# Performance work log

Hardware: AMD Instinct MI355X
Metric: run time of the kernel (lower is better)

Reference implementation:

```python
import jax, jax.numpy as jnp
import numpy as np

KH, KW = 3, 3
T_MIN, T_MAX = 0.0, 1.0  # default layer params (set_params never called)


def setup_inputs() -> dict:
    key = jax.random.key(0)
    k1, k2, k3 = jax.random.split(key, 3)
    # spike times in [0, 1]
    tj = jax.random.uniform(k1, (16, 258, 258), dtype=jnp.float32)
    # (filters, 1, kh, kw), scaled so outputs are not all clamped at t_max
    kernel = jax.random.normal(k2, (128, 1, KH, KW), dtype=jnp.float32) * 0.05
    D_i = jax.random.normal(k3, (9, 128), dtype=jnp.float32) * 0.01
    return {"tj": tj, "kernel": kernel, "D_i": D_i}


def reference(tj, kernel, D_i):
    # tj: [B, S, S]; valid padding, default branch (BN buffer == 0).
    B, S, _ = tj.shape
    Hv = S - KH + 1  # image_valid_size
    Fc = kernel.shape[0]
    # torch: W = kernel.view(-1, filters) -> row-major reinterpretation of (F,1,kh,kw) as (9, F)
    W = kernel.reshape(KH * KW, Fc)
    # 3x3 patches per (batch-as-channel) map, kernel taps in row-major (ki, kj) order
    patches = jnp.stack(
        [tj[:, i:i + Hv, j:j + Hv] for i in range(KH) for j in range(KW)],
        axis=-1,
    )  # [B, Hv, Hv, 9]
    # torch unfold layout: row index = patch_l * B + channel_c
    X = jnp.transpose(patches, (1, 2, 0, 3)).reshape(-1, KH * KW)  # [Hv*Hv*B, 9]
    threshold = (T_MAX - T_MIN) - D_i[0]  # (F,)
    ti = (X - T_MIN) @ W + threshold + T_MIN  # [N, F]
    ti = jnp.where(ti < T_MAX, ti, T_MAX)  # clamp late spikes to t_max
    return ti.reshape(-1, Hv, Hv, Fc)  # matches torch .view(-1, Hv, Hv, F)
```

## Files before the change

kernel.cpp:

```cpp
#include <hip/hip_runtime.h>


#define B_N   16
#define S_N   258
#define HV_N  256
#define F_N   128

#define GRID      8192
#define WPB       4
#define NSTREAM   (GRID * WPB)
#define NTASK     ((HV_N * (HV_N / 4)) * B_N)

typedef float v2f __attribute__((ext_vector_type(2)));

__global__ __launch_bounds__(256, 6) void spiking_conv2d_kernel(
    const float* __restrict__ tj, const float* __restrict__ kern,
    const float* __restrict__ Di, float* __restrict__ out) {
  const int lane = threadIdx.x & 63;
  const int wid  = __builtin_amdgcn_readfirstlane(threadIdx.x >> 6);

  float2 w[9];
#pragma unroll
  for (int t = 0; t < 9; ++t)
    w[t] = reinterpret_cast<const float2*>(kern)[t * (F_N / 2) + lane];
  const float2 d = reinterpret_cast<const float2*>(Di)[lane];
  const float thx = 1.0f - d.x, thy = 1.0f - d.y;

  auto load_task = [&](int t, float (&x)[18]) {
    const int b    = t & (B_N - 1);
    const int pblk = t >> 4;
    const int j0   = (pblk & 63) << 2;
    const int i    = pblk >> 6;
    const float* s = tj + (b * S_N + i) * S_N + j0;
#pragma unroll
    for (int r = 0; r < 3; ++r)
#pragma unroll
      for (int c = 0; c < 6; ++c)
        x[r * 6 + c] = s[r * S_N + c];
  };

  auto compute_store = [&](int t, const float (&x)[18]) {
    const int b    = t & (B_N - 1);
    const int pblk = t >> 4;
    const int j0   = (pblk & 63) << 2;
    const int i    = pblk >> 6;
    const int n0   = ((i * HV_N + j0) << 4) | b;
    v2f* o = reinterpret_cast<v2f*>(out) + (long)n0 * (F_N / 2) + lane;
#pragma unroll
    for (int p = 0; p < 4; ++p) {
      float ax = thx, ay = thy;
#pragma unroll
      for (int r = 0; r < 3; ++r)
#pragma unroll
        for (int c = 0; c < 3; ++c) {
          const float xv = x[r * 6 + p + c];
          ax = fmaf(xv, w[r * 3 + c].x, ax);
          ay = fmaf(xv, w[r * 3 + c].y, ay);
        }
      v2f v = {fminf(ax, 1.0f), fminf(ay, 1.0f)};
      __builtin_nontemporal_store(v, o + p * (16 * (F_N / 2)));
    }
  };

  float xa[18], xb[18];
  int t = blockIdx.x * WPB + wid;
  if (t >= NTASK) return;
  load_task(t, xa);
#pragma unroll 1
  for (; t + NSTREAM < NTASK; ) {
    load_task(t + NSTREAM, xb);
    compute_store(t, xa);
    t += NSTREAM;
    if (t + NSTREAM < NTASK) {
      load_task(t + NSTREAM, xa);
      compute_store(t, xb);
      t += NSTREAM;
    } else {
      compute_store(t, xb);
      t += NSTREAM;
    }
  }
  if (t < NTASK) compute_store(t, xa);
}

extern "C" void kernel_launch(void* const* d_in, const int* in_sizes, int n_in,
                              void* d_out, int out_size, void* d_ws, size_t ws_size,
                              hipStream_t stream) {
  const float* tj   = (const float*)d_in[0];
  const float* kern = (const float*)d_in[1];
  const float* Di   = (const float*)d_in[2];
  float* out = (float*)d_out;
  spiking_conv2d_kernel<<<GRID, 256, 0, stream>>>(tj, kern, Di, out);
}
```

Baseline: 530.1 us.

## Process two batch channels per wave with 16-byte output stores

```diff
diff --git a/kernel.cpp b/kernel.cpp
--- a/kernel.cpp
+++ b/kernel.cpp
@@ -9,60 +9,70 @@
 #define GRID      8192
 #define WPB       4
 #define NSTREAM   (GRID * WPB)
-#define NTASK     ((HV_N * (HV_N / 4)) * B_N)
+#define NTASK     ((HV_N * (HV_N / 4)) * (B_N / 2))
 
-typedef float v2f __attribute__((ext_vector_type(2)));
+typedef float v4f __attribute__((ext_vector_type(4)));
 
 __global__ __launch_bounds__(256, 6) void spiking_conv2d_kernel(
     const float* __restrict__ tj, const float* __restrict__ kern,
     const float* __restrict__ Di, float* __restrict__ out) {
   const int lane = threadIdx.x & 63;
+  const int q    = lane & 31;
+  const bool hi  = lane >= 32;
   const int wid  = __builtin_amdgcn_readfirstlane(threadIdx.x >> 6);
 
-  float2 w[9];
+  float4 w[9];
 #pragma unroll
   for (int t = 0; t < 9; ++t)
-    w[t] = reinterpret_cast<const float2*>(kern)[t * (F_N / 2) + lane];
-  const float2 d = reinterpret_cast<const float2*>(Di)[lane];
-  const float thx = 1.0f - d.x, thy = 1.0f - d.y;
+    w[t] = reinterpret_cast<const float4*>(kern)[t * (F_N / 4) + q];
+  const float4 d = reinterpret_cast<const float4*>(Di)[q];
+  const float4 thr = make_float4(1.0f - d.x, 1.0f - d.y, 1.0f - d.z, 1.0f - d.w);
 
-  auto load_task = [&](int t, float (&x)[18]) {
-    const int b    = t & (B_N - 1);
-    const int pblk = t >> 4;
+  auto load_task = [&](int t, float (&x)[36]) {
+    const int bp   = t & 7;
+    const int pblk = t >> 3;
     const int j0   = (pblk & 63) << 2;
     const int i    = pblk >> 6;
-    const float* s = tj + (b * S_N + i) * S_N + j0;
 #pragma unroll
-    for (int r = 0; r < 3; ++r)
-#pragma unroll
-      for (int c = 0; c < 6; ++c)
-        x[r * 6 + c] = s[r * S_N + c];
-  };
-
-  auto compute_store = [&](int t, const float (&x)[18]) {
-    const int b    = t & (B_N - 1);
-    const int pblk = t >> 4;
-    const int j0   = (pblk & 63) << 2;
-    const int i    = pblk >> 6;
-    const int n0   = ((i * HV_N + j0) << 4) | b;
-    v2f* o = reinterpret_cast<v2f*>(out) + (long)n0 * (F_N / 2) + lane;
-#pragma unroll
-    for (int p = 0; p < 4; ++p) {
-      float ax = thx, ay = thy;
+    for (int h = 0; h < 2; ++h) {
+      const float* s = tj + ((2 * bp + h) * S_N + i) * S_N + j0;
 #pragma unroll
       for (int r = 0; r < 3; ++r)
 #pragma unroll
-        for (int c = 0; c < 3; ++c) {
-          const float xv = x[r * 6 + p + c];
-          ax = fmaf(xv, w[r * 3 + c].x, ax);
-          ay = fmaf(xv, w[r * 3 + c].y, ay);
-        }
-      v2f v = {fminf(ax, 1.0f), fminf(ay, 1.0f)};
-      __builtin_nontemporal_store(v, o + p * (16 * (F_N / 2)));
+        for (int c = 0; c < 6; ++c)
+          x[h * 18 + r * 6 + c] = s[r * S_N + c];
     }
   };
 
-  float xa[18], xb[18];
+  auto compute_store = [&](int t, const float (&x)[36]) {
+    const int bp   = t & 7;
+    const int pblk = t >> 3;
+    const int j0   = (pblk & 63) << 2;
+    const int i    = pblk >> 6;
+    const int n0   = ((i * HV_N + j0) << 4) + 2 * bp;
+    v4f* o = reinterpret_cast<v4f*>(out) + (long)n0 * (F_N / 4) + lane;
+#pragma unroll
+    for (int p = 0; p < 4; ++p) {
+      float xv[9];
+#pragma unroll
+      for (int r = 0; r < 3; ++r)
+#pragma unroll
+        for (int c = 0; c < 3; ++c)
+          xv[r * 3 + c] = hi ? x[18 + r * 6 + p + c] : x[r * 6 + p + c];
+      float ax = thr.x, ay = thr.y, az = thr.z, aw = thr.w;
+#pragma unroll
+      for (int k = 0; k < 9; ++k) {
+        ax = fmaf(xv[k], w[k].x, ax);
+        ay = fmaf(xv[k], w[k].y, ay);
+        az = fmaf(xv[k], w[k].z, az);
+        aw = fmaf(xv[k], w[k].w, aw);
+      }
+      v4f v = {fminf(ax, 1.0f), fminf(ay, 1.0f), fminf(az, 1.0f), fminf(aw, 1.0f)};
+      __builtin_nontemporal_store(v, o + p * (16 * (F_N / 4)));
+    }
+  };
+
+  float xa[36], xb[36];
   int t = blockIdx.x * WPB + wid;
   if (t >= NTASK) return;
   load_task(t, xa);
```

New measurement: 558.8 us. 1.05x slower.
